# Optimization experiments

Hardware: AMD Instinct MI355X
Metric: run time of the kernel (lower is better)

## Reference

```python
import jax, jax.numpy as jnp
import numpy as np

N_NODES = 100000
N_EDGES = 1600000
SZ_IN = 128
DIM_I = 1024


def setup_inputs() -> dict:
    key = jax.random.key(0)
    k1, k2, k3, k4, k5 = jax.random.split(key, 5)
    x = jax.random.normal(k1, (N_NODES, SZ_IN), dtype=jnp.float32)
    edge_index = jax.random.randint(k2, (2, N_EDGES), 0, N_NODES, dtype=jnp.int64)
    # torch Linear weight is [out_features, in_features]
    agg_W = jax.random.normal(k3, (SZ_IN, SZ_IN), dtype=jnp.float32) / np.sqrt(SZ_IN)
    agg_b = jnp.zeros((SZ_IN,), dtype=jnp.float32)
    lin_W = jax.random.normal(k4, (DIM_I, 2 * SZ_IN), dtype=jnp.float32) / np.sqrt(2 * SZ_IN)
    return {"x": x, "edge_index": edge_index, "agg_W": agg_W, "agg_b": agg_b, "lin_W": lin_W}


def reference(x, edge_index, agg_W, agg_b, lin_W):
    # GraphSAGE layer, depth=1, agg='max', concat=True, training mode (no self-loop/dropout edits).
    u, v = edge_index[0], edge_index[1]
    n = x.shape[0]
    # gather neighbor features, linear + ReLU  -> [E, sz_in]
    msg = jax.nn.relu(x[v] @ agg_W.T + agg_b)
    # scatter-max per target node; torch_scatter initializes out to zeros,
    # so missing nodes get 0 and all results are max(values, 0)
    hn = jnp.maximum(jax.ops.segment_max(msg, u, num_segments=n), 0.0)
    # concat + linear (no bias) + ReLU -> [N, dim_i]
    h = jax.nn.relu(jnp.concatenate([x, hn], axis=1) @ lin_W.T)
    return h
```

## Files before the change

### kernel.cpp

```cpp
#include <hip/hip_runtime.h>
#include <hip/hip_bf16.h>

typedef __attribute__((ext_vector_type(8))) short short8;
typedef __attribute__((ext_vector_type(4))) float f32x4;

__device__ __forceinline__ float bfu2f(unsigned short u) {
    unsigned int x = ((unsigned int)u) << 16;
    float f;
    __builtin_memcpy(&f, &x, 4);
    return f;
}
__device__ __forceinline__ unsigned short f2bfu(float f) {
    unsigned int x;
    __builtin_memcpy(&x, &f, 4);
    unsigned int r = (x + 0x7FFFu + ((x >> 16) & 1u)) >> 16;
    return (unsigned short)r;
}

__device__ __forceinline__ void gload_lds16(const void* g, void* l) {
    __builtin_amdgcn_global_load_lds(
        (const __attribute__((address_space(1))) void*)g,
        (__attribute__((address_space(3))) void*)l, 16, 0, 0);
}

#define BM 128
#define BN 128
#define BK 32
#define LDA 32

template<bool F32OUT>
__global__ __launch_bounds__(256, 2)
void gemm_bt(const unsigned short* __restrict__ Alo,
             const unsigned short* __restrict__ Ahi,
             const unsigned short* __restrict__ B,
             const float* __restrict__ bias,
             void* __restrict__ Cv,
             int M, int N, int K, int relu)
{
    __shared__ unsigned short As[BM * LDA];
    __shared__ unsigned short Bs[BN * LDA];

    const int tid  = threadIdx.x;
    const int nwg  = gridDim.x * gridDim.y;
    int lid = blockIdx.y * gridDim.x + blockIdx.x;
    int wg  = lid;
    if ((nwg & 7) == 0) {
        int cpx = nwg >> 3;
        wg = (lid & 7) * cpx + (lid >> 3);
    }
    const int m0 = (wg / gridDim.x) * BM;
    const int n0 = (wg % gridDim.x) * BN;

    const int lane = tid & 63;
    const int wave = tid >> 6;
    const int wr   = wave >> 1;
    const int wc   = wave & 1;
    const int fm   = lane & 15;
    const int fq   = lane >> 4;

    f32x4 acc[4][4] = {};

    const int wbase = tid & ~63;

    for (int k0 = 0; k0 < K; k0 += BK) {
        __syncthreads();
        const unsigned short* Ab = (k0 < 128) ? Alo : Ahi;
        const int ka = (k0 < 128) ? k0 : (k0 - 128);
        #pragma unroll
        for (int i = 0; i < 2; ++i) {
            int c  = i * 256 + tid;
            int r  = c >> 2;
            int c8 = (c & 3) << 3;
            int grow = m0 + r;
            if (grow >= M) grow = M - 1;
            gload_lds16(Ab + (size_t)grow * 128 + ka + c8,
                        &As[(i * 256 + wbase) * 8]);
            gload_lds16(B + (size_t)(n0 + r) * K + k0 + c8,
                        &Bs[(i * 256 + wbase) * 8]);
        }
        __syncthreads();

        short8 af[4], bf[4];
        #pragma unroll
        for (int i = 0; i < 4; ++i)
            af[i] = *(const short8*)(&As[(wr * 64 + i * 16 + fm) * LDA + fq * 8]);
        #pragma unroll
        for (int j = 0; j < 4; ++j)
            bf[j] = *(const short8*)(&Bs[(wc * 64 + j * 16 + fm) * LDA + fq * 8]);

        #pragma unroll
        for (int i = 0; i < 4; ++i)
            #pragma unroll
            for (int j = 0; j < 4; ++j)
                acc[i][j] = __builtin_amdgcn_mfma_f32_16x16x32_bf16(
                                af[i], bf[j], acc[i][j], 0, 0, 0);
    }

    #pragma unroll
    for (int i = 0; i < 4; ++i) {
        #pragma unroll
        for (int r = 0; r < 4; ++r) {
            int gm = m0 + wr * 64 + i * 16 + fq * 4 + r;
            if (gm < M) {
                #pragma unroll
                for (int j = 0; j < 4; ++j) {
                    int gn = n0 + wc * 64 + j * 16 + fm;
                    float val = acc[i][j][r];
                    if (bias) val += bias[gn];
                    if (relu) val = fmaxf(val, 0.0f);
                    if (F32OUT)
                        ((float*)Cv)[(size_t)gm * N + gn] = val;
                    else
                        ((unsigned short*)Cv)[(size_t)gm * N + gn] = f2bfu(val);
                }
            }
        }
    }
}

__global__ __launch_bounds__(256)
void cvt_k(const float* __restrict__ src, unsigned short* __restrict__ dst, int n4)
{
    int t = blockIdx.x * 256 + threadIdx.x;
    if (t >= n4) return;
    float4 f = ((const float4*)src)[t];
    ushort4 o;
    o.x = f2bfu(f.x); o.y = f2bfu(f.y); o.z = f2bfu(f.z); o.w = f2bfu(f.w);
    ((ushort4*)dst)[t] = o;
}

__global__ __launch_bounds__(256)
void deg_k(const int* __restrict__ ei, int* __restrict__ deg, int E)
{
    int e = (blockIdx.x * 256 + threadIdx.x) * 4;
    if (e >= E) return;
    if (e + 3 < E) {
        int4 u = *(const int4*)(ei + e);
        atomicAdd(&deg[u.x], 1);
        atomicAdd(&deg[u.y], 1);
        atomicAdd(&deg[u.z], 1);
        atomicAdd(&deg[u.w], 1);
    } else {
        for (int j = 0; j < 4 && e + j < E; ++j) atomicAdd(&deg[ei[e + j]], 1);
    }
}

__global__ __launch_bounds__(256)
void scan1_k(const int* __restrict__ deg, int* __restrict__ bsum, int NN)
{
    __shared__ int s[256];
    int t = threadIdx.x;
    int base = blockIdx.x * 1024 + t * 4;
    int sum = 0;
    if (base + 3 < NN) {
        int4 d = *(const int4*)(deg + base);
        sum = d.x + d.y + d.z + d.w;
    } else {
        for (int j = 0; j < 4; ++j) if (base + j < NN) sum += deg[base + j];
    }
    s[t] = sum;
    __syncthreads();
    for (int ofs = 128; ofs > 0; ofs >>= 1) {
        if (t < ofs) s[t] += s[t + ofs];
        __syncthreads();
    }
    if (t == 0) bsum[blockIdx.x] = s[0];
}

__global__ __launch_bounds__(256)
void scan2_k(int* __restrict__ bsum, int* __restrict__ offN, int NB)
{
    __shared__ int s[256];
    int t = threadIdx.x;
    int v = (t < NB) ? bsum[t] : 0;
    s[t] = v;
    __syncthreads();
    for (int ofs = 1; ofs < 256; ofs <<= 1) {
        int w = (t >= ofs) ? s[t - ofs] : 0;
        __syncthreads();
        s[t] += w;
        __syncthreads();
    }
    if (t < NB) bsum[t] = (t > 0) ? s[t - 1] : 0;
    if (t == 255) *offN = s[255];
}

__global__ __launch_bounds__(256)
void scan3_k(const int* __restrict__ deg, const int* __restrict__ bsum,
             int* __restrict__ off, int* __restrict__ cur, int NN)
{
    __shared__ int s[256];
    int t = threadIdx.x;
    int base = blockIdx.x * 1024 + t * 4;
    int d0 = 0, d1 = 0, d2 = 0, d3 = 0;
    if (base + 3 < NN) {
        int4 d = *(const int4*)(deg + base);
        d0 = d.x; d1 = d.y; d2 = d.z; d3 = d.w;
    } else {
        if (base     < NN) d0 = deg[base];
        if (base + 1 < NN) d1 = deg[base + 1];
        if (base + 2 < NN) d2 = deg[base + 2];
        if (base + 3 < NN) d3 = deg[base + 3];
    }
    s[t] = d0 + d1 + d2 + d3;
    __syncthreads();
    for (int ofs = 1; ofs < 256; ofs <<= 1) {
        int w = (t >= ofs) ? s[t - ofs] : 0;
        __syncthreads();
        s[t] += w;
        __syncthreads();
    }
    int o0 = bsum[blockIdx.x] + ((t > 0) ? s[t - 1] : 0);
    int o1 = o0 + d0, o2 = o1 + d1, o3 = o2 + d2;
    if (base + 3 < NN) {
        *(int4*)(off + base) = make_int4(o0, o1, o2, o3);
        *(int4*)(cur + base) = make_int4(o0, o1, o2, o3);
    } else {
        if (base     < NN) { off[base]     = o0; cur[base]     = o0; }
        if (base + 1 < NN) { off[base + 1] = o1; cur[base + 1] = o1; }
        if (base + 2 < NN) { off[base + 2] = o2; cur[base + 2] = o2; }
        if (base + 3 < NN) { off[base + 3] = o3; cur[base + 3] = o3; }
    }
}

__global__ __launch_bounds__(256)
void fill_k(const int* __restrict__ ei, int* __restrict__ cur,
            int* __restrict__ adj, int E)
{
    int e = (blockIdx.x * 256 + threadIdx.x) * 2;
    if (e >= E) return;
    if (e + 1 < E) {
        int2 u2 = *(const int2*)(ei + e);
        int2 v2 = *(const int2*)(ei + E + e);
        int p0 = atomicAdd(&cur[u2.x], 1); adj[p0] = v2.x;
        int p1 = atomicAdd(&cur[u2.y], 1); adj[p1] = v2.y;
    } else {
        int u = ei[e], v = ei[E + e];
        int p = atomicAdd(&cur[u], 1); adj[p] = v;
    }
}

__global__ __launch_bounds__(256)
void gather_max_k(const int* __restrict__ off, const int* __restrict__ adj,
                  const unsigned short* __restrict__ y,
                  unsigned short* __restrict__ hnb, int NN)
{
    int t = blockIdx.x * 256 + threadIdx.x;
    int u = t >> 4;
    if (u >= NN) return;
    int c = (t & 15) << 3;
    int s = off[u], e2 = off[u + 1];
    float a[8] = {0.f, 0.f, 0.f, 0.f, 0.f, 0.f, 0.f, 0.f};
    int i = s;
    for (; i + 1 < e2; i += 2) {
        int v0 = adj[i], v1 = adj[i + 1];
        short8 ya = *(const short8*)(y + (size_t)v0 * 128 + c);
        short8 yb = *(const short8*)(y + (size_t)v1 * 128 + c);
        #pragma unroll
        for (int j = 0; j < 8; ++j)
            a[j] = fmaxf(a[j], fmaxf(bfu2f((unsigned short)ya[j]),
                                     bfu2f((unsigned short)yb[j])));
    }
    if (i < e2) {
        int v0 = adj[i];
        short8 ya = *(const short8*)(y + (size_t)v0 * 128 + c);
        #pragma unroll
        for (int j = 0; j < 8; ++j)
            a[j] = fmaxf(a[j], bfu2f((unsigned short)ya[j]));
    }
    short8 o;
    #pragma unroll
    for (int j = 0; j < 8; ++j) o[j] = (short)f2bfu(a[j]);
    *(short8*)(hnb + (size_t)u * 128 + c) = o;
}

extern "C" void kernel_launch(void* const* d_in, const int* in_sizes, int n_in,
                              void* d_out, int out_size, void* d_ws, size_t ws_size,
                              hipStream_t stream)
{
    const float* x     = (const float*)d_in[0];
    const int*   ei    = (const int*)d_in[1];
    const float* agg_W = (const float*)d_in[2];
    const float* agg_b = (const float*)d_in[3];
    const float* lin_W = (const float*)d_in[4];
    float*       out   = (float*)d_out;

    const int NN = in_sizes[0] / 128;
    const int E  = in_sizes[1] / 2;
    const int DI = in_sizes[4] / 256;

    char* ws = (char*)d_ws;
    const size_t xN = (size_t)NN * 128;
    unsigned short* xb  = (unsigned short*)ws;
    unsigned short* y   = xb + xN;
    unsigned short* hnb = y + xN;
    unsigned short* awb = hnb + xN;
    unsigned short* lwb = awb + 128 * 128;
    char* p = (char*)(lwb + (size_t)DI * 256);
    int* deg = (int*)p;
    int* off = deg + NN;
    int* cur = off + NN + 1;
    int* adj = cur + NN;
    int* bsum = adj + E;

    const int MT = (NN + BM - 1) / BM;
    const int NB = (NN + 1023) / 1024;

    cvt_k<<<((int)(xN / 4) + 255) / 256, 256, 0, stream>>>(x, xb, (int)(xN / 4));
    cvt_k<<<(128 * 128 / 4 + 255) / 256, 256, 0, stream>>>(agg_W, awb, 128 * 128 / 4);
    cvt_k<<<(DI * 256 / 4 + 255) / 256, 256, 0, stream>>>(lin_W, lwb, DI * 256 / 4);

    gemm_bt<false><<<dim3(1, MT), 256, 0, stream>>>(xb, xb, awb, agg_b, y, NN, 128, 128, 0);

    hipMemsetAsync(deg, 0, (size_t)NN * sizeof(int), stream);
    deg_k<<<(E / 4 + 255) / 256, 256, 0, stream>>>(ei, deg, E);
    scan1_k<<<NB, 256, 0, stream>>>(deg, bsum, NN);
    scan2_k<<<1, 256, 0, stream>>>(bsum, off + NN, NB);
    scan3_k<<<NB, 256, 0, stream>>>(deg, bsum, off, cur, NN);
    fill_k<<<(E / 2 + 255) / 256, 256, 0, stream>>>(ei, cur, adj, E);

    {
        long long threads = (long long)NN * 16;
        int blocks = (int)((threads + 255) / 256);
        gather_max_k<<<blocks, 256, 0, stream>>>(off, adj, y, hnb, NN);
    }

    gemm_bt<true><<<dim3(DI / BN, MT), 256, 0, stream>>>(xb, hnb, lwb, nullptr, out, NN, DI, 256, 1);
}
```

Measured before the change: 786.2 us.

## Fuse conversions and degree zeroing, bf16-native max gather, nontemporal output stores

Merges the three fp32-to-bf16 conversion kernels and the degree memset into a single prep kernel, removing launch overhead. The gather-max now compares bf16 bit patterns directly as shorts with a 4-way unroll and two accumulators, dropping the float conversions. Fill processes four edges per thread, and the final GEMM writes its fp32 output with nontemporal stores to keep the large output out of cache. Comparing bf16 values as signed shorts is only valid because values are non-negative after the ReLU and the zero initialisation; negative zero or NaN would order differently.

```diff
diff --git a/kernel.cpp b/kernel.cpp
--- a/kernel.cpp
+++ b/kernel.cpp
@@ -109,7 +109,8 @@
                     if (bias) val += bias[gn];
                     if (relu) val = fmaxf(val, 0.0f);
                     if (F32OUT)
-                        ((float*)Cv)[(size_t)gm * N + gn] = val;
+                        __builtin_nontemporal_store(val,
+                            &((float*)Cv)[(size_t)gm * N + gn]);
                     else
                         ((unsigned short*)Cv)[(size_t)gm * N + gn] = f2bfu(val);
                 }
@@ -118,15 +119,29 @@
     }
 }
 
-__global__ __launch_bounds__(256)
-void cvt_k(const float* __restrict__ src, unsigned short* __restrict__ dst, int n4)
-{
-    int t = blockIdx.x * 256 + threadIdx.x;
-    if (t >= n4) return;
+__device__ __forceinline__ void cvt4(const float* __restrict__ src,
+                                     unsigned short* __restrict__ dst, int t)
+{
     float4 f = ((const float4*)src)[t];
     ushort4 o;
     o.x = f2bfu(f.x); o.y = f2bfu(f.y); o.z = f2bfu(f.z); o.w = f2bfu(f.w);
     ((ushort4*)dst)[t] = o;
+}
+
+__global__ __launch_bounds__(256)
+void prep_k(const float* __restrict__ x, unsigned short* __restrict__ xb, int n4x,
+            const float* __restrict__ aW, unsigned short* __restrict__ awb, int n4a,
+            const float* __restrict__ lW, unsigned short* __restrict__ lwb, int n4l,
+            int* __restrict__ deg, int n4d)
+{
+    int t = blockIdx.x * 256 + threadIdx.x;
+    if (t < n4x) { cvt4(x, xb, t); return; }
+    t -= n4x;
+    if (t < n4a) { cvt4(aW, awb, t); return; }
+    t -= n4a;
+    if (t < n4l) { cvt4(lW, lwb, t); return; }
+    t -= n4l;
+    if (t < n4d) ((int4*)deg)[t] = make_int4(0, 0, 0, 0);
 }
 
 __global__ __launch_bounds__(256)
@@ -227,16 +242,20 @@
 void fill_k(const int* __restrict__ ei, int* __restrict__ cur,
             int* __restrict__ adj, int E)
 {
-    int e = (blockIdx.x * 256 + threadIdx.x) * 2;
+    int e = (blockIdx.x * 256 + threadIdx.x) * 4;
     if (e >= E) return;
-    if (e + 1 < E) {
-        int2 u2 = *(const int2*)(ei + e);
-        int2 v2 = *(const int2*)(ei + E + e);
-        int p0 = atomicAdd(&cur[u2.x], 1); adj[p0] = v2.x;
-        int p1 = atomicAdd(&cur[u2.y], 1); adj[p1] = v2.y;
-    } else {
-        int u = ei[e], v = ei[E + e];
-        int p = atomicAdd(&cur[u], 1); adj[p] = v;
+    if (e + 3 < E) {
+        int4 u = *(const int4*)(ei + e);
+        int4 v = *(const int4*)(ei + E + e);
+        int p0 = atomicAdd(&cur[u.x], 1); adj[p0] = v.x;
+        int p1 = atomicAdd(&cur[u.y], 1); adj[p1] = v.y;
+        int p2 = atomicAdd(&cur[u.z], 1); adj[p2] = v.z;
+        int p3 = atomicAdd(&cur[u.w], 1); adj[p3] = v.w;
+    } else {
+        for (int j = 0; j < 4 && e + j < E; ++j) {
+            int u = ei[e + j], v = ei[E + e + j];
+            int p = atomicAdd(&cur[u], 1); adj[p] = v;
+        }
     }
 }
 
@@ -249,29 +268,28 @@
     int u = t >> 4;
     if (u >= NN) return;
     int c = (t & 15) << 3;
+    const unsigned short* yc = y + c;
     int s = off[u], e2 = off[u + 1];
-    float a[8] = {0.f, 0.f, 0.f, 0.f, 0.f, 0.f, 0.f, 0.f};
+    short8 a0 = {0, 0, 0, 0, 0, 0, 0, 0};
+    short8 a1 = {0, 0, 0, 0, 0, 0, 0, 0};
     int i = s;
-    for (; i + 1 < e2; i += 2) {
-        int v0 = adj[i], v1 = adj[i + 1];
-        short8 ya = *(const short8*)(y + (size_t)v0 * 128 + c);
-        short8 yb = *(const short8*)(y + (size_t)v1 * 128 + c);
-        #pragma unroll
-        for (int j = 0; j < 8; ++j)
-            a[j] = fmaxf(a[j], fmaxf(bfu2f((unsigned short)ya[j]),
-                                     bfu2f((unsigned short)yb[j])));
-    }
-    if (i < e2) {
-        int v0 = adj[i];
-        short8 ya = *(const short8*)(y + (size_t)v0 * 128 + c);
-        #pragma unroll
-        for (int j = 0; j < 8; ++j)
-            a[j] = fmaxf(a[j], bfu2f((unsigned short)ya[j]));
-    }
-    short8 o;
-    #pragma unroll
-    for (int j = 0; j < 8; ++j) o[j] = (short)f2bfu(a[j]);
-    *(short8*)(hnb + (size_t)u * 128 + c) = o;
+    for (; i + 3 < e2; i += 4) {
+        int v0 = adj[i], v1 = adj[i + 1], v2 = adj[i + 2], v3 = adj[i + 3];
+        short8 y0 = *(const short8*)(yc + (size_t)v0 * 128);
+        short8 y1 = *(const short8*)(yc + (size_t)v1 * 128);
+        short8 y2 = *(const short8*)(yc + (size_t)v2 * 128);
+        short8 y3 = *(const short8*)(yc + (size_t)v3 * 128);
+        a0 = __builtin_elementwise_max(a0, y0);
+        a1 = __builtin_elementwise_max(a1, y1);
+        a0 = __builtin_elementwise_max(a0, y2);
+        a1 = __builtin_elementwise_max(a1, y3);
+    }
+    for (; i < e2; ++i) {
+        short8 y0 = *(const short8*)(yc + (size_t)adj[i] * 128);
+        a0 = __builtin_elementwise_max(a0, y0);
+    }
+    a0 = __builtin_elementwise_max(a0, a1);
+    *(short8*)(hnb + (size_t)u * 128 + c) = a0;
 }
 
 extern "C" void kernel_launch(void* const* d_in, const int* in_sizes, int n_in,
@@ -306,18 +324,23 @@
     const int MT = (NN + BM - 1) / BM;
     const int NB = (NN + 1023) / 1024;
 
-    cvt_k<<<((int)(xN / 4) + 255) / 256, 256, 0, stream>>>(x, xb, (int)(xN / 4));
-    cvt_k<<<(128 * 128 / 4 + 255) / 256, 256, 0, stream>>>(agg_W, awb, 128 * 128 / 4);
-    cvt_k<<<(DI * 256 / 4 + 255) / 256, 256, 0, stream>>>(lin_W, lwb, DI * 256 / 4);
+    const int n4x = (int)(xN / 4);
+    const int n4a = 128 * 128 / 4;
+    const int n4l = DI * 256 / 4;
+    const int n4d = (NN + 3) / 4;
+    {
+        long long tot = (long long)n4x + n4a + n4l + n4d;
+        prep_k<<<(int)((tot + 255) / 256), 256, 0, stream>>>(
+            x, xb, n4x, agg_W, awb, n4a, lin_W, lwb, n4l, deg, n4d);
+    }
 
     gemm_bt<false><<<dim3(1, MT), 256, 0, stream>>>(xb, xb, awb, agg_b, y, NN, 128, 128, 0);
 
-    hipMemsetAsync(deg, 0, (size_t)NN * sizeof(int), stream);
     deg_k<<<(E / 4 + 255) / 256, 256, 0, stream>>>(ei, deg, E);
     scan1_k<<<NB, 256, 0, stream>>>(deg, bsum, NN);
     scan2_k<<<1, 256, 0, stream>>>(bsum, off + NN, NB);
     scan3_k<<<NB, 256, 0, stream>>>(deg, bsum, off, cur, NN);
-    fill_k<<<(E / 2 + 255) / 256, 256, 0, stream>>>(ei, cur, adj, E);
+    fill_k<<<(E / 4 + 255) / 256, 256, 0, stream>>>(ei, cur, adj, E);
 
     {
         long long threads = (long long)NN * 16;
```

New measurement: 753.7 us. 4.1% less time.
